# Performance work log

Measured on AMD Instinct MI355X. Metric: run time of the kernel, lower is better.

## Reference

```python
import jax, jax.numpy as jnp
import numpy as np

EPS = 1e-12  # F.normalize default eps

def _l2norm(x):
    return x / jnp.maximum(jnp.linalg.norm(x, axis=-1, keepdims=True), EPS)

def setup_inputs() -> dict:
    key = jax.random.key(0)
    k1, k2, k3 = jax.random.split(key, 3)
    N, C, D = 131072, 1000, 256
    feat = jax.random.normal(k1, (N, D), dtype=jnp.float32)
    # memory bank is initialized to L2-normalized centers in the original (init())
    memory = _l2norm(jax.random.normal(k2, (C, D), dtype=jnp.float32))
    label = jax.random.randint(k3, (N,), 0, C, dtype=jnp.int64)
    return {"feat": feat, "memory": memory, "label": label}

def reference(feat, memory, label):
    num_cls, feat_dim = memory.shape
    N = feat.shape[0]
    t = 1.0  # forward default temperature

    featn = _l2norm(feat)

    # --- update(feat, label): fused per-class masked gather+sum as one segment_sum ---
    f = jax.lax.stop_gradient(featn)  # feat.detach() in original
    sums = jax.ops.segment_sum(f, label, num_segments=num_cls)          # [C, D]
    counts = jax.ops.segment_sum(jnp.ones((N,), f.dtype), label, num_segments=num_cls)
    flags = (counts > 0).astype(f.dtype)[:, None]                        # [C, 1]
    batch_center = _l2norm(sums) * flags                                 # zeros for empty classes

    # --- update_center_by_simi ---
    simi = jnp.sum(memory * batch_center, axis=-1, keepdims=True)        # [C, 1]
    update_wei = 1.0 - (1.0 - simi) * flags                              # [C, 1]
    new_memory = _l2norm(update_wei * memory + (1.0 - update_wei) * batch_center)

    # --- similarity + cross entropy ---
    simis = jnp.einsum('nd,cd->nc', featn, new_memory) / t               # [N, C]
    logp = jax.nn.log_softmax(simis, axis=-1)
    loss = -jnp.mean(jnp.take_along_axis(logp, label[:, None], axis=1))
    return loss
```

## Files before the change

### kernel.cpp

```cpp
#include <hip/hip_runtime.h>

#define NROWS 131072
#define NCLS  1000
#define CPAD  1024
#define DDIM  256

typedef __attribute__((ext_vector_type(8))) short bf16x8;
typedef __attribute__((ext_vector_type(4))) float f32x4;
typedef __attribute__((ext_vector_type(4))) unsigned u32x4;

__device__ __forceinline__ float wred(float v){
#pragma unroll
  for (int m = 1; m < 64; m <<= 1) v += __shfl_xor(v, m, 64);
  return v;
}

__device__ __forceinline__ ushort f2bf(float x){
  union { float f; unsigned u; } c; c.f = x;
  return (ushort)((c.u + 0x7FFFu + ((c.u >> 16) & 1u)) >> 16);
}

__device__ __forceinline__ float fexp2(float x){
#if __has_builtin(__builtin_amdgcn_exp2f)
  return __builtin_amdgcn_exp2f(x);
#else
  float r; asm("v_exp_f32 %0, %1" : "=v"(r) : "v"(x)); return r;
#endif
}

__device__ __forceinline__ void store_frag(ushort* nmem, int c, int ln, ushort4 v){
  int ch = c >> 5, nb = (c >> 4) & 1, r16 = c & 15;
  int k = ln >> 3, g = (ln >> 1) & 3, half = ln & 1;
  *(ushort4*)(nmem + ch*8192 + (k*2+nb)*512 + (g*16+r16)*8 + half*4) = v;
}

__global__ __launch_bounds__(1024) void k_center(
    const float* __restrict__ feat, const float* __restrict__ memory,
    const int* __restrict__ label, ushort* __restrict__ nmem){
  const int c0 = blockIdx.x * 2;
  const int t = threadIdx.x;
  const int w = t >> 6, lane = t & 63;
  if (c0 >= NCLS){
    if (t < 128) store_frag(nmem, c0 + (t >> 6), t & 63, make_ushort4(0,0,0,0));
    return;
  }
  const int c1 = c0 + 1;
  __shared__ float4 accred[2][16][64];
  __shared__ int cw[2][16];

  float4 a0 = make_float4(0.f,0.f,0.f,0.f);
  float4 a1 = make_float4(0.f,0.f,0.f,0.f);
  int cnt0 = 0, cnt1 = 0;
  const float4* feat4 = (const float4*)feat;
  const int4*   lab4  = (const int4*)label;

  for (int it = 0; it < 32; ++it){
    int base = (w*32 + it) * 256;
    int4 lv = lab4[base/4 + lane];
#pragma unroll
    for (int sub = 0; sub < 4; ++sub){
      int lvv = (sub==0)?lv.x:(sub==1)?lv.y:(sub==2)?lv.z:lv.w;
      unsigned long long m0 = __ballot(lvv == c0);
      unsigned long long m1 = __ballot(lvv == c1);
      cnt0 += (int)__popcll(m0); cnt1 += (int)__popcll(m1);
      while (m0){
        int b = __ffsll((long long)m0) - 1; m0 &= m0 - 1;
        int r = base + b*4 + sub;
        float4 x = feat4[r*64 + lane];
        float ss = wred(x.x*x.x + x.y*x.y + x.z*x.z + x.w*x.w);
        float sc = 1.0f / fmaxf(sqrtf(ss), 1e-12f);
        a0.x += x.x*sc; a0.y += x.y*sc; a0.z += x.z*sc; a0.w += x.w*sc;
      }
      while (m1){
        int b = __ffsll((long long)m1) - 1; m1 &= m1 - 1;
        int r = base + b*4 + sub;
        float4 x = feat4[r*64 + lane];
        float ss = wred(x.x*x.x + x.y*x.y + x.z*x.z + x.w*x.w);
        float sc = 1.0f / fmaxf(sqrtf(ss), 1e-12f);
        a1.x += x.x*sc; a1.y += x.y*sc; a1.z += x.z*sc; a1.w += x.w*sc;
      }
    }
  }
  accred[0][w][lane] = a0; accred[1][w][lane] = a1;
  if (lane == 0){ cw[0][w] = cnt0; cw[1][w] = cnt1; }
  __syncthreads();

  if (t < 128){
    int cls = t >> 6, ln = t & 63;
    float sx=0.f, sy=0.f, sz=0.f, sw=0.f; int total = 0;
#pragma unroll
    for (int s = 0; s < 16; ++s){
      float4 v = accred[cls][s][ln];
      sx += v.x; sy += v.y; sz += v.z; sw += v.w;
      total += cw[cls][s];
    }
    int c = c0 + cls;
    float ss = wred(sx*sx + sy*sy + sz*sz + sw*sw);
    float inv = 1.0f / fmaxf(sqrtf(ss), 1e-12f);
    float bx = sx*inv, by = sy*inv, bz = sz*inv, bw = sw*inv;
    float flag = (total > 0) ? 1.0f : 0.0f;
    float4 m = ((const float4*)memory)[c*64 + ln];
    float simi = wred(m.x*bx + m.y*by + m.z*bz + m.w*bw);
    float wei = 1.0f - (1.0f - simi)*flag;
    float rx = wei*m.x + (1.0f-wei)*bx;
    float ry = wei*m.y + (1.0f-wei)*by;
    float rz = wei*m.z + (1.0f-wei)*bz;
    float rw = wei*m.w + (1.0f-wei)*bw;
    float ss2 = wred(rx*rx + ry*ry + rz*rz + rw*rw);
    float inv2 = 1.0f / fmaxf(sqrtf(ss2), 1e-12f);
    store_frag(nmem, c, ln,
        make_ushort4(f2bf(rx*inv2), f2bf(ry*inv2), f2bf(rz*inv2), f2bf(rw*inv2)));
  }
}

#define MFMA16 __builtin_amdgcn_mfma_f32_16x16x32_bf16

__global__ __launch_bounds__(256, 2) void k_gemm(
    const float* __restrict__ feat, const ushort* __restrict__ nmem,
    const int* __restrict__ label, float* __restrict__ partials){
  __shared__ float bred[4];
  const int t = threadIdx.x, w = t >> 6, lane = t & 63;
  const int g = lane >> 4, r16 = lane & 15;
  const int rowbase = blockIdx.x * 128;

  bf16x8 areg[2][8];
  float rs_self[2];
#pragma unroll
  for (int mf = 0; mf < 2; ++mf){
    int row = rowbase + w*32 + mf*16 + r16;
    const float4* rp = (const float4*)(feat + row*DDIM);
    float ss = 0.f;
#pragma unroll
    for (int kt = 0; kt < 8; ++kt){
      float4 x0 = rp[kt*8 + g*2];
      float4 x1 = rp[kt*8 + g*2 + 1];
      ss += x0.x*x0.x + x0.y*x0.y + x0.z*x0.z + x0.w*x0.w
          + x1.x*x1.x + x1.y*x1.y + x1.z*x1.z + x1.w*x1.w;
      u32x4 pk;
      pk[0] = (__float_as_uint(x0.y) & 0xFFFF0000u) | (__float_as_uint(x0.x) >> 16);
      pk[1] = (__float_as_uint(x0.w) & 0xFFFF0000u) | (__float_as_uint(x0.z) >> 16);
      pk[2] = (__float_as_uint(x1.y) & 0xFFFF0000u) | (__float_as_uint(x1.x) >> 16);
      pk[3] = (__float_as_uint(x1.w) & 0xFFFF0000u) | (__float_as_uint(x1.z) >> 16);
      areg[mf][kt] = __builtin_bit_cast(bf16x8, pk);
    }
    ss += __shfl_xor(ss, 16, 64);
    ss += __shfl_xor(ss, 32, 64);
    rs_self[mf] = 1.0f / fmaxf(sqrtf(ss), 1e-12f);
  }

  int labreg[2][4];
  float rs2[2][4];
#pragma unroll
  for (int m = 0; m < 2; ++m)
#pragma unroll
    for (int j = 0; j < 4; ++j){
      int rr = w*32 + m*16 + g*4 + j;
      labreg[m][j] = label[rowbase + rr];
      rs2[m][j] = __shfl(rs_self[m], g*4 + j, 16) * 1.44269504f;
    }

  float esum[2][4] = {{0.f,0.f,0.f,0.f},{0.f,0.f,0.f,0.f}};
  float slb [2][4] = {{0.f,0.f,0.f,0.f},{0.f,0.f,0.f,0.f}};

  const char* nb = (const char*)nmem + lane*16;

  for (int ch = 0; ch < 32; ++ch){
    const char* cb = nb + (size_t)ch*16384;
    bf16x8 b0[8], b1[8];
#pragma unroll
    for (int k = 0; k < 8; ++k){
      b0[k] = *(const bf16x8*)(cb + (k*2+0)*1024);
      b1[k] = *(const bf16x8*)(cb + (k*2+1)*1024);
    }

    f32x4 acc[2][2];
    __builtin_amdgcn_s_setprio(1);
    {
      f32x4 Z = {0.f,0.f,0.f,0.f};
      acc[0][0] = MFMA16(areg[0][0], b0[0], Z, 0, 0, 0);
      acc[0][1] = MFMA16(areg[0][0], b1[0], Z, 0, 0, 0);
      acc[1][0] = MFMA16(areg[1][0], b0[0], Z, 0, 0, 0);
      acc[1][1] = MFMA16(areg[1][0], b1[0], Z, 0, 0, 0);
    }
#pragma unroll
    for (int k = 1; k < 8; ++k){
      acc[0][0] = MFMA16(areg[0][k], b0[k], acc[0][0], 0, 0, 0);
      acc[0][1] = MFMA16(areg[0][k], b1[k], acc[0][1], 0, 0, 0);
      acc[1][0] = MFMA16(areg[1][k], b0[k], acc[1][0], 0, 0, 0);
      acc[1][1] = MFMA16(areg[1][k], b1[k], acc[1][1], 0, 0, 0);
    }
    __builtin_amdgcn_s_setprio(0);

#pragma unroll
    for (int m = 0; m < 2; ++m)
#pragma unroll
      for (int n = 0; n < 2; ++n){
        int col = ch*32 + n*16 + r16;
#pragma unroll
        for (int j = 0; j < 4; ++j){
          float v = acc[m][n][j] * rs2[m][j];
          esum[m][j] += fexp2(v);
          slb[m][j]  += (col == labreg[m][j]) ? v : 0.f;
        }
      }
  }

  float v = 0.f;
#pragma unroll
  for (int m = 0; m < 2; ++m)
#pragma unroll
    for (int j = 0; j < 4; ++j){
      float e = esum[m][j], s = slb[m][j];
      e += __shfl_xor(e, 1, 64); e += __shfl_xor(e, 2, 64);
      e += __shfl_xor(e, 4, 64); e += __shfl_xor(e, 8, 64);
      s += __shfl_xor(s, 1, 64); s += __shfl_xor(s, 2, 64);
      s += __shfl_xor(s, 4, 64); s += __shfl_xor(s, 8, 64);
      v += 0.69314718056f * (__log2f(e - 24.0f) - s);
    }
  if (r16 != 0) v = 0.f;
  v = wred(v);
  if (lane == 0) bred[w] = v;
  __syncthreads();
  if (t == 0) partials[blockIdx.x] = bred[0] + bred[1] + bred[2] + bred[3];
}

__global__ __launch_bounds__(256) void k_final(
    const float* __restrict__ partials, float* __restrict__ out){
  const int t = threadIdx.x;
  const int w = t >> 6, lane = t & 63;
  __shared__ float red[4];
  float s = partials[t] + partials[t+256] + partials[t+512] + partials[t+768];
  s = wred(s);
  if (lane == 0) red[w] = s;
  __syncthreads();
  if (t == 0) out[0] = (red[0]+red[1]+red[2]+red[3]) * (1.0f/(float)NROWS);
}

extern "C" void kernel_launch(void* const* d_in, const int* in_sizes, int n_in,
                              void* d_out, int out_size, void* d_ws, size_t ws_size,
                              hipStream_t stream){
  const float* feat   = (const float*)d_in[0];
  const float* memory = (const float*)d_in[1];
  const int*   label  = (const int*)d_in[2];
  float* out = (float*)d_out;
  ushort* nmem = (ushort*)d_ws;
  float* partials = (float*)((char*)d_ws + (size_t)CPAD*DDIM*2);

  k_center<<<CPAD/2, 1024, 0, stream>>>(feat, memory, label, nmem);
  k_gemm<<<NROWS/128, 256, 0, stream>>>(feat, nmem, label, partials);
  k_final<<<1, 256, 0, stream>>>(partials, out);
}
```

Before: 134.9 us.

## Double-buffer B fragment loads across chunks and rotate chunk start per block

The GEMM loop now splits each chunk's B fragments into low and high K halves. It prefetches the next chunk's halves right after the MFMAs that consume the current half, so global or L2 load latency overlaps with compute instead of stalling at the top of each iteration. Each block also starts at a different chunk (rotated by block index) to spread L2 and channel traffic over the memory buffer. The label-logit accumulation becomes a select instead of an add. The risks are higher register pressure under launch_bounds(256,2) and a compiler that may not schedule the loads early.

```diff
diff --git a/kernel.cpp b/kernel.cpp
--- a/kernel.cpp
+++ b/kernel.cpp
@@ -162,45 +162,70 @@
   float esum[2][4] = {{0.f,0.f,0.f,0.f},{0.f,0.f,0.f,0.f}};
   float slb [2][4] = {{0.f,0.f,0.f,0.f},{0.f,0.f,0.f,0.f}};
 
-  const char* nb = (const char*)nmem + lane*16;
-
-  for (int ch = 0; ch < 32; ++ch){
-    const char* cb = nb + (size_t)ch*16384;
-    bf16x8 b0[8], b1[8];
-#pragma unroll
-    for (int k = 0; k < 8; ++k){
-      b0[k] = *(const bf16x8*)(cb + (k*2+0)*1024);
-      b1[k] = *(const bf16x8*)(cb + (k*2+1)*1024);
-    }
+  const char* nbp = (const char*)nmem + lane*16;
+  const int rot = blockIdx.x & 31;
+  bf16x8 bA[8], bB[8];
+
+#define LOADLO(CH)                                                            \
+  { const char* cb = nbp + (size_t)(CH)*16384;                                \
+    _Pragma("unroll")                                                         \
+    for (int i = 0; i < 8; ++i) bA[i] = *(const bf16x8*)(cb + i*1024); }
+#define LOADHI(CH)                                                            \
+  { const char* cb = nbp + (size_t)(CH)*16384 + 8192;                         \
+    _Pragma("unroll")                                                         \
+    for (int i = 0; i < 8; ++i) bB[i] = *(const bf16x8*)(cb + i*1024); }
+
+  {
+    int c0 = rot;
+    LOADLO(c0); LOADHI(c0);
+  }
+
+  for (int it = 0; it < 32; ++it){
+    int cur = (it + rot) & 31;
+    int nxt = (it + 1 + rot) & 31;
 
     f32x4 acc[2][2];
     __builtin_amdgcn_s_setprio(1);
     {
       f32x4 Z = {0.f,0.f,0.f,0.f};
-      acc[0][0] = MFMA16(areg[0][0], b0[0], Z, 0, 0, 0);
-      acc[0][1] = MFMA16(areg[0][0], b1[0], Z, 0, 0, 0);
-      acc[1][0] = MFMA16(areg[1][0], b0[0], Z, 0, 0, 0);
-      acc[1][1] = MFMA16(areg[1][0], b1[0], Z, 0, 0, 0);
-    }
-#pragma unroll
-    for (int k = 1; k < 8; ++k){
-      acc[0][0] = MFMA16(areg[0][k], b0[k], acc[0][0], 0, 0, 0);
-      acc[0][1] = MFMA16(areg[0][k], b1[k], acc[0][1], 0, 0, 0);
-      acc[1][0] = MFMA16(areg[1][k], b0[k], acc[1][0], 0, 0, 0);
-      acc[1][1] = MFMA16(areg[1][k], b1[k], acc[1][1], 0, 0, 0);
+      acc[0][0] = MFMA16(areg[0][0], bA[0], Z, 0, 0, 0);
+      acc[0][1] = MFMA16(areg[0][0], bA[1], Z, 0, 0, 0);
+      acc[1][0] = MFMA16(areg[1][0], bA[0], Z, 0, 0, 0);
+      acc[1][1] = MFMA16(areg[1][0], bA[1], Z, 0, 0, 0);
+    }
+#pragma unroll
+    for (int k = 1; k < 4; ++k){
+      acc[0][0] = MFMA16(areg[0][k], bA[k*2+0], acc[0][0], 0, 0, 0);
+      acc[0][1] = MFMA16(areg[0][k], bA[k*2+1], acc[0][1], 0, 0, 0);
+      acc[1][0] = MFMA16(areg[1][k], bA[k*2+0], acc[1][0], 0, 0, 0);
+      acc[1][1] = MFMA16(areg[1][k], bA[k*2+1], acc[1][1], 0, 0, 0);
     }
     __builtin_amdgcn_s_setprio(0);
 
+    if (it < 31) LOADLO(nxt);
+
+    __builtin_amdgcn_s_setprio(1);
+#pragma unroll
+    for (int k = 4; k < 8; ++k){
+      acc[0][0] = MFMA16(areg[0][k], bB[(k-4)*2+0], acc[0][0], 0, 0, 0);
+      acc[0][1] = MFMA16(areg[0][k], bB[(k-4)*2+1], acc[0][1], 0, 0, 0);
+      acc[1][0] = MFMA16(areg[1][k], bB[(k-4)*2+0], acc[1][0], 0, 0, 0);
+      acc[1][1] = MFMA16(areg[1][k], bB[(k-4)*2+1], acc[1][1], 0, 0, 0);
+    }
+    __builtin_amdgcn_s_setprio(0);
+
+    if (it < 31) LOADHI(nxt);
+
 #pragma unroll
     for (int m = 0; m < 2; ++m)
 #pragma unroll
       for (int n = 0; n < 2; ++n){
-        int col = ch*32 + n*16 + r16;
+        int col = cur*32 + n*16 + r16;
 #pragma unroll
         for (int j = 0; j < 4; ++j){
           float v = acc[m][n][j] * rs2[m][j];
           esum[m][j] += fexp2(v);
-          slb[m][j]  += (col == labreg[m][j]) ? v : 0.f;
+          slb[m][j] = (col == labreg[m][j]) ? v : slb[m][j];
         }
       }
   }
```

Result: faster. 129.9 us (-3.7%).
